# Performance work log

Hardware: AMD Instinct MI355X
Metric: run time of the kernel (lower is better)

The kernel has to match this reference:

```python
import jax, jax.numpy as jnp
import numpy as np

N_NODES = 100000
N_EDGES = 1600000
IN_FEATS = 128
HEADS = 8
OUT_FEATS = 16
NEG_SLOPE = 0.2


def setup_inputs() -> dict:
    key = jax.random.key(0)
    ks = jax.random.split(key, 7)
    feats = jax.random.normal(ks[0], (N_NODES, IN_FEATS), dtype=jnp.float32)
    W = jax.random.normal(ks[1], (IN_FEATS, HEADS * OUT_FEATS), dtype=jnp.float32) * (1.0 / np.sqrt(IN_FEATS))
    attn_l = jax.random.normal(ks[2], (HEADS, OUT_FEATS), dtype=jnp.float32) * 0.1
    attn_r = jax.random.normal(ks[3], (HEADS, OUT_FEATS), dtype=jnp.float32) * 0.1
    bias_vec = jax.random.normal(ks[4], (HEADS * OUT_FEATS,), dtype=jnp.float32) * 0.01
    src = jax.random.randint(ks[5], (N_EDGES,), 0, N_NODES, dtype=jnp.int32)
    dst = jax.random.randint(ks[6], (N_EDGES,), 0, N_NODES, dtype=jnp.int32)
    return {"feats": feats, "W": W, "attn_l": attn_l, "attn_r": attn_r,
            "bias_vec": bias_vec, "src": src, "dst": dst}


def reference(feats, W, attn_l, attn_r, bias_vec, src, dst):
    N = feats.shape[0]
    H, D = attn_l.shape
    # linear projection (feat_drop = 0 in eval): [N, H, D]
    h = (feats @ W).reshape(N, H, D)
    # per-node attention halves: [N, H]
    el = jnp.einsum('nhd,hd->nh', h, attn_l)
    er = jnp.einsum('nhd,hd->nh', h, attn_r)
    # per-edge score with LeakyReLU: [E, H]
    e = jax.nn.leaky_relu(el[src] + er[dst], negative_slope=NEG_SLOPE)
    # edge softmax segmented by destination node
    seg_max = jax.ops.segment_max(e, dst, num_segments=N)            # [N, H]
    seg_max = jnp.where(jnp.isfinite(seg_max), seg_max, 0.0)          # zero-in-degree guard
    exp_e = jnp.exp(e - seg_max[dst])                                 # [E, H]
    seg_sum = jax.ops.segment_sum(exp_e, dst, num_segments=N)        # [N, H]
    alpha = exp_e / seg_sum[dst]                                      # [E, H]
    # weighted gather-scatter aggregation: [N, H, D]
    msg = alpha[:, :, None] * h[src]
    rst = jax.ops.segment_sum(msg, dst, num_segments=N)
    # identity residual (in_feats == H*D) + bias, then flatten
    rst = rst + h + bias_vec.reshape(1, H, D)
    return rst.reshape(N, H * D)
```

## Files before the change

kernel.cpp:

```cpp
#include <hip/hip_runtime.h>

#define NEG 0.2f
#define CHUNK 2048
#define BINW 48

using bf16x8 = __attribute__((ext_vector_type(8))) short;
using f32x4  = __attribute__((ext_vector_type(4))) float;
using f32x2  = __attribute__((ext_vector_type(2))) float;
using u32x4  = __attribute__((ext_vector_type(4))) unsigned int;

__device__ __forceinline__ short f2bf(float f) {
    union { float f; unsigned u; } v; v.f = f;
    unsigned r = v.u + 0x7FFFu + ((v.u >> 16) & 1u);
    return (short)(r >> 16);
}
__device__ __forceinline__ float bflo(unsigned v) {
    union { unsigned u; float f; } x; x.u = v << 16; return x.f;
}
__device__ __forceinline__ float bfhi(unsigned v) {
    union { unsigned u; float f; } x; x.u = v & 0xffff0000u; return x.f;
}

__global__ __launch_bounds__(256) void k_wt(const float* __restrict__ W,
                                            unsigned short* __restrict__ Wbf,
                                            int* __restrict__ cnt, int N) {
    int idx = (blockIdx.x * 256 + threadIdx.x) * 4;
    #pragma unroll
    for (int q = 0; q < 4; ++q) {
        int i = idx + q;
        int k = i >> 7, c = i & 127;
        Wbf[c * 128 + k] = (unsigned short)f2bf(W[i]);
    }
    for (int i = blockIdx.x * 256 + threadIdx.x; i < N; i += gridDim.x * 256)
        cnt[i] = 0;
}

__global__ __launch_bounds__(256) void k_fill(const int* __restrict__ src,
                                              const int* __restrict__ dst,
                                              int* __restrict__ cnt,
                                              int* __restrict__ bins,
                                              int E, int N8) {
    int b = blockIdx.x;
    int r = b & 7;
    int c = b >> 3;
    int lo = r * N8, hi = lo + N8;
    int base = c * CHUNK + threadIdx.x;
    #pragma unroll
    for (int q = 0; q < 8; ++q) {
        int e = base + q * 256;
        if (e < E) {
            int d = __builtin_nontemporal_load(dst + e);
            if (d >= lo && d < hi) {
                int s = __builtin_nontemporal_load(src + e);
                int p = atomicAdd(&cnt[d], 1);
                if (p < BINW) bins[(size_t)d * BINW + p] = s;
            }
        }
    }
}

__global__ __launch_bounds__(256) void k_gemm(const float* __restrict__ feats,
                                              const unsigned short* __restrict__ Wbf,
                                              unsigned short* __restrict__ h,
                                              const float* __restrict__ attn_l,
                                              const float* __restrict__ attn_r,
                                              float* __restrict__ el,
                                              float* __restrict__ er,
                                              unsigned char* __restrict__ h8,
                                              int N) {
    __shared__ __align__(16) short Wt[128 * 136];
    const int t = threadIdx.x;
    const int n0 = blockIdx.x * 64;

    {
        const uint4* Ws = (const uint4*)Wbf;
        #pragma unroll
        for (int i = 0; i < 8; ++i) {
            int g = t * 8 + i;
            int c = g >> 4, j = g & 15;
            *(uint4*)&Wt[c * 136 + j * 8] = Ws[g];
        }
    }
    __syncthreads();

    const int w    = t >> 6;
    const int lane = t & 63;
    const int m    = lane & 15;
    const int quad = lane >> 4;
    const int kq   = quad * 8;

    const int row_a = n0 + w * 16 + m;
    const bool va = (row_a < N);

    f32x4 acc[8];
    #pragma unroll
    for (int ti = 0; ti < 8; ++ti) acc[ti] = (f32x4){0.f, 0.f, 0.f, 0.f};

    #pragma unroll
    for (int kc = 0; kc < 4; ++kc) {
        const f32x4* ap = (const f32x4*)(feats + (size_t)row_a * 128 + kc * 32 + kq);
        f32x4 a0 = (f32x4){0.f,0.f,0.f,0.f}, a1 = (f32x4){0.f,0.f,0.f,0.f};
        if (va) {
            a0 = __builtin_nontemporal_load(ap);
            a1 = __builtin_nontemporal_load(ap + 1);
        }
        bf16x8 af;
        af[0] = f2bf(a0[0]); af[1] = f2bf(a0[1]); af[2] = f2bf(a0[2]); af[3] = f2bf(a0[3]);
        af[4] = f2bf(a1[0]); af[5] = f2bf(a1[1]); af[6] = f2bf(a1[2]); af[7] = f2bf(a1[3]);
        #pragma unroll
        for (int ti = 0; ti < 8; ++ti) {
            bf16x8 bf = *(const bf16x8*)&Wt[(ti * 16 + m) * 136 + kc * 32 + kq];
            acc[ti] = __builtin_amdgcn_mfma_f32_16x16x32_bf16(af, bf, acc[ti], 0, 0, 0);
        }
    }

    __syncthreads();
    short* hs = Wt;
    const int row_l = w * 16 + quad * 4;
    #pragma unroll
    for (int ti = 0; ti < 8; ++ti) {
        int col = ti * 16 + m;
        #pragma unroll
        for (int r = 0; r < 4; ++r)
            hs[(row_l + r) * 136 + col] = f2bf(acc[ti][r]);
    }
    __syncthreads();

    #pragma unroll
    for (int u = 0; u < 2; ++u) {
        int p = u * 256 + t;
        int row = p >> 3, hd = p & 7;
        int rg = n0 + row;
        if (rg < N) {
            const uint4* hp = (const uint4*)&hs[row * 136 + hd * 16];
            uint4 u0 = hp[0], u1 = hp[1];

            uint4* hg = (uint4*)(h + (size_t)rg * 128 + hd * 16);
            hg[0] = u0; hg[1] = u1;

            float hv[16];
            hv[0]=bflo(u0.x); hv[1]=bfhi(u0.x); hv[2]=bflo(u0.y); hv[3]=bfhi(u0.y);
            hv[4]=bflo(u0.z); hv[5]=bfhi(u0.z); hv[6]=bflo(u0.w); hv[7]=bfhi(u0.w);
            hv[8]=bflo(u1.x); hv[9]=bfhi(u1.x); hv[10]=bflo(u1.y); hv[11]=bfhi(u1.y);
            hv[12]=bflo(u1.z); hv[13]=bfhi(u1.z); hv[14]=bflo(u1.w); hv[15]=bfhi(u1.w);

            unsigned p0 = 0, p1 = 0, p2 = 0, p3 = 0;
            p0 = __builtin_amdgcn_cvt_pk_fp8_f32(hv[0],  hv[1],  p0, false);
            p0 = __builtin_amdgcn_cvt_pk_fp8_f32(hv[2],  hv[3],  p0, true);
            p1 = __builtin_amdgcn_cvt_pk_fp8_f32(hv[4],  hv[5],  p1, false);
            p1 = __builtin_amdgcn_cvt_pk_fp8_f32(hv[6],  hv[7],  p1, true);
            p2 = __builtin_amdgcn_cvt_pk_fp8_f32(hv[8],  hv[9],  p2, false);
            p2 = __builtin_amdgcn_cvt_pk_fp8_f32(hv[10], hv[11], p2, true);
            p3 = __builtin_amdgcn_cvt_pk_fp8_f32(hv[12], hv[13], p3, false);
            p3 = __builtin_amdgcn_cvt_pk_fp8_f32(hv[14], hv[15], p3, true);
            *(uint4*)(h8 + (size_t)rg * 128 + hd * 16) = make_uint4(p0, p1, p2, p3);

            const float4* al = (const float4*)(attn_l + hd * 16);
            const float4* ar = (const float4*)(attn_r + hd * 16);
            float sl = 0.f, sr = 0.f;
            #pragma unroll
            for (int q = 0; q < 4; ++q) {
                float4 a = al[q], b = ar[q];
                sl += hv[4*q]*a.x + hv[4*q+1]*a.y + hv[4*q+2]*a.z + hv[4*q+3]*a.w;
                sr += hv[4*q]*b.x + hv[4*q+1]*b.y + hv[4*q+2]*b.z + hv[4*q+3]*b.w;
            }
            el[rg * 8 + hd] = sl;
            er[rg * 8 + hd] = sr;
        }
    }
}

__global__ __launch_bounds__(256) void k_agg(const int* __restrict__ cnt,
                                             const int* __restrict__ bins,
                                             const float* __restrict__ el,
                                             const float* __restrict__ er,
                                             const unsigned char* __restrict__ h8,
                                             const unsigned short* __restrict__ h,
                                             const float* __restrict__ bias,
                                             float* __restrict__ out, int N) {
    int nb = gridDim.x;
    int b  = blockIdx.x;
    int g  = ((nb & 7) == 0) ? ((b & 7) * (nb >> 3) + (b >> 3)) : b;

    int t = threadIdx.x;
    int n = g * 4 + (t >> 6);
    if (n >= N) return;
    int lane = t & 63;
    int q    = lane >> 4;
    int c16  = lane & 15;
    int hd   = c16 >> 1;
    int deg  = cnt[n];
    if (deg > BINW) deg = BINW;
    int begin = n * BINW;
    int end   = begin + deg;
    float erv = er[n * 8 + hd];

    float acc[8] = {0.f,0.f,0.f,0.f,0.f,0.f,0.f,0.f};
    float expsum = 0.f;

    auto edge = [&](int p) {
        int s = __builtin_nontemporal_load(bins + p);
        float x = el[s * 8 + hd] + erv;
        x = x > 0.f ? x : NEG * x;
        float w = __expf(x);
        expsum += w;
        uint2 hv = *(const uint2*)(h8 + (size_t)s * 128 + c16 * 8);
        f32x2 d0 = __builtin_amdgcn_cvt_pk_f32_fp8(hv.x, false);
        f32x2 d1 = __builtin_amdgcn_cvt_pk_f32_fp8(hv.x, true);
        f32x2 d2 = __builtin_amdgcn_cvt_pk_f32_fp8(hv.y, false);
        f32x2 d3 = __builtin_amdgcn_cvt_pk_f32_fp8(hv.y, true);
        acc[0] += w * d0[0]; acc[1] += w * d0[1];
        acc[2] += w * d1[0]; acc[3] += w * d1[1];
        acc[4] += w * d2[0]; acc[5] += w * d2[1];
        acc[6] += w * d3[0]; acc[7] += w * d3[1];
    };

    int p = begin + q;
    for (; p + 12 < end; p += 16) { edge(p); edge(p + 4); edge(p + 8); edge(p + 12); }
    for (; p < end; p += 4) edge(p);

    #pragma unroll
    for (int k = 0; k < 8; ++k) {
        acc[k] += __shfl_xor(acc[k], 32);
        acc[k] += __shfl_xor(acc[k], 16);
    }
    expsum += __shfl_xor(expsum, 32);
    expsum += __shfl_xor(expsum, 16);

    if (q == 0) {
        float inv = expsum > 0.f ? 1.f / expsum : 0.f;
        u32x4 hn = __builtin_nontemporal_load((const u32x4*)(h + (size_t)n * 128 + c16 * 8));
        const float4* bp = (const float4*)(bias + c16 * 8);
        float4 b0 = bp[0], b1 = bp[1];
        f32x4 o0, o1;
        o0[0] = acc[0]*inv + bflo(hn[0]) + b0.x;
        o0[1] = acc[1]*inv + bfhi(hn[0]) + b0.y;
        o0[2] = acc[2]*inv + bflo(hn[1]) + b0.z;
        o0[3] = acc[3]*inv + bfhi(hn[1]) + b0.w;
        o1[0] = acc[4]*inv + bflo(hn[2]) + b1.x;
        o1[1] = acc[5]*inv + bfhi(hn[2]) + b1.y;
        o1[2] = acc[6]*inv + bflo(hn[3]) + b1.z;
        o1[3] = acc[7]*inv + bfhi(hn[3]) + b1.w;
        f32x4* op = (f32x4*)(out + (size_t)n * 128 + c16 * 8);
        __builtin_nontemporal_store(o0, op);
        __builtin_nontemporal_store(o1, op + 1);
    }
}

extern "C" void kernel_launch(void* const* d_in, const int* in_sizes, int n_in,
                              void* d_out, int out_size, void* d_ws, size_t ws_size,
                              hipStream_t stream) {
    const float* feats  = (const float*)d_in[0];
    const float* W      = (const float*)d_in[1];
    const float* attn_l = (const float*)d_in[2];
    const float* attn_r = (const float*)d_in[3];
    const float* bias   = (const float*)d_in[4];
    const int*   src    = (const int*)d_in[5];
    const int*   dst    = (const int*)d_in[6];

    const int N  = in_sizes[0] / 128;
    const int E  = in_sizes[5];
    const int N8 = (N + 7) / 8;
    const int CH = (E + CHUNK - 1) / CHUNK;
    const int GB = (N + 63) / 64;

    float* out = (float*)d_out;
    char*  ws  = (char*)d_ws;
    unsigned short* Wbf = (unsigned short*)ws;         ws += 128 * 128 * 2;
    unsigned short* h = (unsigned short*)ws;           ws += (size_t)N * 128 * 2;
    unsigned char* h8 = (unsigned char*)ws;            ws += (size_t)N * 128;
    float* el      = (float*)ws;                       ws += (size_t)N * 8 * 4;
    float* er      = (float*)ws;                       ws += (size_t)N * 8 * 4;
    int*   cnt     = (int*)ws;                         ws += (size_t)N * 4;
    int*   bins    = (int*)ws;                         ws += (size_t)N * BINW * 4;

    k_wt   <<<16,           256, 0, stream>>>(W, Wbf, cnt, N);
    k_gemm <<<GB,           256, 0, stream>>>(feats, Wbf, h, attn_l, attn_r, el, er, h8, N);
    k_fill <<<CH * 8,       256, 0, stream>>>(src, dst, cnt, bins, E, N8);
    k_agg  <<<(N + 3) / 4,  256, 0, stream>>>(cnt, bins, el, er, h8, h, bias, out, N);
}
```

Measured before the change: 282.0 us.

## Merge edge binning and projection GEMM into one heterogeneous launch

Combines the edge-binning fill kernel and the projection GEMM kernel into a single launch. The first FB blocks do the binning and the remaining blocks do the GEMM, so the two independent stages can run concurrently and one launch is removed. The GEMM blocks grow to 512 threads covering 128 rows, which halves the number of W tile loads into shared memory. In exchange, the shared-memory allocation is now reserved for fill blocks that never use it, which can lower their occupancy. The GEMM and fill blocks also compete for memory bandwidth.

```diff
diff --git a/kernel.cpp b/kernel.cpp
--- a/kernel.cpp
+++ b/kernel.cpp
@@ -1,7 +1,6 @@
 #include <hip/hip_runtime.h>
 
 #define NEG 0.2f
-#define CHUNK 2048
 #define BINW 48
 
 using bf16x8 = __attribute__((ext_vector_type(8))) short;
@@ -35,56 +34,61 @@
         cnt[i] = 0;
 }
 
-__global__ __launch_bounds__(256) void k_fill(const int* __restrict__ src,
-                                              const int* __restrict__ dst,
-                                              int* __restrict__ cnt,
-                                              int* __restrict__ bins,
-                                              int E, int N8) {
-    int b = blockIdx.x;
-    int r = b & 7;
-    int c = b >> 3;
-    int lo = r * N8, hi = lo + N8;
-    int base = c * CHUNK + threadIdx.x;
-    #pragma unroll
-    for (int q = 0; q < 8; ++q) {
-        int e = base + q * 256;
-        if (e < E) {
-            int d = __builtin_nontemporal_load(dst + e);
-            if (d >= lo && d < hi) {
-                int s = __builtin_nontemporal_load(src + e);
-                int p = atomicAdd(&cnt[d], 1);
-                if (p < BINW) bins[(size_t)d * BINW + p] = s;
+__global__ __launch_bounds__(512) void k_fg(const float* __restrict__ feats,
+                                            const unsigned short* __restrict__ Wbf,
+                                            unsigned short* __restrict__ h,
+                                            const float* __restrict__ attn_l,
+                                            const float* __restrict__ attn_r,
+                                            float* __restrict__ el,
+                                            float* __restrict__ er,
+                                            unsigned char* __restrict__ h8,
+                                            const int* __restrict__ src,
+                                            const int* __restrict__ dst,
+                                            int* __restrict__ cnt,
+                                            int* __restrict__ bins,
+                                            int N, int E, int N8, int FB) {
+    __shared__ __align__(16) short Wt[128 * 136];
+
+    if (blockIdx.x < FB) {
+        int b = blockIdx.x;
+        int r = b & 7;
+        int c = b >> 3;
+        int lo = r * N8, hi = lo + N8;
+        int base = c * 4096 + threadIdx.x;
+        #pragma unroll
+        for (int q = 0; q < 8; ++q) {
+            int e = base + q * 512;
+            if (e < E) {
+                int d = __builtin_nontemporal_load(dst + e);
+                if (d >= lo && d < hi) {
+                    int s = __builtin_nontemporal_load(src + e);
+                    int p = atomicAdd(&cnt[d], 1);
+                    if (p < BINW) bins[(size_t)d * BINW + p] = s;
+                }
             }
         }
-    }
-}
-
-__global__ __launch_bounds__(256) void k_gemm(const float* __restrict__ feats,
-                                              const unsigned short* __restrict__ Wbf,
-                                              unsigned short* __restrict__ h,
-                                              const float* __restrict__ attn_l,
-                                              const float* __restrict__ attn_r,
-                                              float* __restrict__ el,
-                                              float* __restrict__ er,
-                                              unsigned char* __restrict__ h8,
-                                              int N) {
-    __shared__ __align__(16) short Wt[128 * 136];
-    const int t = threadIdx.x;
-    const int n0 = blockIdx.x * 64;
+        return;
+    }
+
+    const int t   = threadIdx.x;
+    const int gb  = blockIdx.x - FB;
+    const int sub = t >> 8;
+    const int tl  = t & 255;
+    const int n0  = gb * 128 + sub * 64;
 
     {
         const uint4* Ws = (const uint4*)Wbf;
         #pragma unroll
-        for (int i = 0; i < 8; ++i) {
-            int g = t * 8 + i;
+        for (int i = 0; i < 4; ++i) {
+            int g = t * 4 + i;
             int c = g >> 4, j = g & 15;
             *(uint4*)&Wt[c * 136 + j * 8] = Ws[g];
         }
     }
     __syncthreads();
 
-    const int w    = t >> 6;
-    const int lane = t & 63;
+    const int w    = tl >> 6;
+    const int lane = tl & 63;
     const int m    = lane & 15;
     const int quad = lane >> 4;
     const int kq   = quad * 8;
@@ -115,24 +119,24 @@
     }
 
     __syncthreads();
-    short* hs = Wt;
+    short* hsb = Wt + sub * (64 * 136);
     const int row_l = w * 16 + quad * 4;
     #pragma unroll
     for (int ti = 0; ti < 8; ++ti) {
         int col = ti * 16 + m;
         #pragma unroll
         for (int r = 0; r < 4; ++r)
-            hs[(row_l + r) * 136 + col] = f2bf(acc[ti][r]);
+            hsb[(row_l + r) * 136 + col] = f2bf(acc[ti][r]);
     }
     __syncthreads();
 
     #pragma unroll
     for (int u = 0; u < 2; ++u) {
-        int p = u * 256 + t;
-        int row = p >> 3, hd = p & 7;
-        int rg = n0 + row;
+        int pp = u * 512 + t;
+        int row128 = pp >> 3, hd = pp & 7;
+        int rg = gb * 128 + row128;
         if (rg < N) {
-            const uint4* hp = (const uint4*)&hs[row * 136 + hd * 16];
+            const uint4* hp = (const uint4*)&Wt[row128 * 136 + hd * 16];
             uint4 u0 = hp[0], u1 = hp[1];
 
             uint4* hg = (uint4*)(h + (size_t)rg * 128 + hd * 16);
@@ -261,8 +265,8 @@
     const int N  = in_sizes[0] / 128;
     const int E  = in_sizes[5];
     const int N8 = (N + 7) / 8;
-    const int CH = (E + CHUNK - 1) / CHUNK;
-    const int GB = (N + 63) / 64;
+    const int FB = ((E + 4095) / 4096) * 8;
+    const int GB = (N + 127) / 128;
 
     float* out = (float*)d_out;
     char*  ws  = (char*)d_ws;
@@ -274,8 +278,8 @@
     int*   cnt     = (int*)ws;                         ws += (size_t)N * 4;
     int*   bins    = (int*)ws;                         ws += (size_t)N * BINW * 4;
 
-    k_wt   <<<16,           256, 0, stream>>>(W, Wbf, cnt, N);
-    k_gemm <<<GB,           256, 0, stream>>>(feats, Wbf, h, attn_l, attn_r, el, er, h8, N);
-    k_fill <<<CH * 8,       256, 0, stream>>>(src, dst, cnt, bins, E, N8);
-    k_agg  <<<(N + 3) / 4,  256, 0, stream>>>(cnt, bins, el, er, h8, h, bias, out, N);
-}
+    k_wt  <<<16,           256, 0, stream>>>(W, Wbf, cnt, N);
+    k_fg  <<<FB + GB,      512, 0, stream>>>(feats, Wbf, h, attn_l, attn_r, el, er, h8,
+                                             src, dst, cnt, bins, N, E, N8, FB);
+    k_agg <<<(N + 3) / 4,  256, 0, stream>>>(cnt, bins, el, er, h8, h, bias, out, N);
+}
```

New measurement: 267.7 us (median of 2 runs). 5.1% less time.
